# Performance work log

Hardware: AMD Instinct MI355X
Metric: run time of the kernel (lower is better)

Reference implementation:

```python
import jax, jax.numpy as jnp
import numpy as np

NODE_IN = 128
NODE_OUT = 128
LEAKY_SLOPE = 0.01  # torch nn.LeakyReLU default


def setup_inputs() -> dict:
    key = jax.random.key(0)
    k1, k2, k3, k4 = jax.random.split(key, 4)
    B, N = 64, 1024
    node_mat = jax.random.normal(k1, (B, N, NODE_IN), dtype=jnp.float32)
    adj_mat = jax.random.uniform(k2, (B, N, N), dtype=jnp.float32)
    # Linear(node_in_len, node_out_len): W [out, in], b [out] (torch default init style)
    bound = 1.0 / np.sqrt(NODE_IN)
    W = jax.random.uniform(k3, (NODE_OUT, NODE_IN), minval=-bound, maxval=bound, dtype=jnp.float32)
    b = jax.random.uniform(k4, (NODE_OUT,), minval=-bound, maxval=bound, dtype=jnp.float32)
    return {"node_mat": node_mat, "adj_mat": adj_mat, "W": W, "b": b}


def reference(node_mat, adj_mat, W, b):
    # n_neighbors[b,i] = sum_j adj[b,i,j]; diag(1/deg) @ adj == adj / deg (row-wise)
    deg = jnp.sum(adj_mat, axis=-1, keepdims=True)          # [B,N,1]
    norm_adj = adj_mat / deg                                 # [B,N,N]
    agg = jnp.einsum('bij,bjf->bif', norm_adj, node_mat)     # [B,N,Fin]
    out = jnp.einsum('bif,of->bio', agg, W) + b              # [B,N,Fout]
    return jnp.where(out >= 0, out, LEAKY_SLOPE * out)
```

## Files before the change

### kernel.cpp

```cpp
#include <hip/hip_runtime.h>
#include <hip/hip_bf16.h>


typedef __attribute__((ext_vector_type(8))) short bf16x8;
typedef __attribute__((ext_vector_type(4))) float f32x4;

__device__ __forceinline__ unsigned f2bf(float x) {
  unsigned u = __builtin_bit_cast(unsigned, x);
  u += 0x7FFFu + ((u >> 16) & 1u);
  return u >> 16;
}
__device__ __forceinline__ int f2bf2(float x, float y) {
  return (int)(f2bf(x) | (f2bf(y) << 16));
}

#define JPAD 136
#define KP   72

__global__ __launch_bounds__(256) void k_ht(const float* __restrict__ node,
                                            const float* __restrict__ W,
                                            ushort* __restrict__ Ht) {
  __shared__ short nt[128 * JPAD];
  __shared__ short wt[128 * JPAD];
  const int b = blockIdx.y, jt = blockIdx.x, t = threadIdx.x;
  const float4* nbase = (const float4*)(node + (size_t)(b * 1024 + jt * 128) * 128);
  const float4* wbase = (const float4*)W;

  #pragma unroll
  for (int p = 0; p < 16; p++) {
    int idx = t + 256 * p;
    int r = idx >> 5, c4 = idx & 31;
    float4 v = nbase[idx];
    int2 s; s.x = f2bf2(v.x, v.y); s.y = f2bf2(v.z, v.w);
    *(int2*)&nt[r * JPAD + c4 * 4] = s;
    float4 wv = wbase[idx];
    int2 sw; sw.x = f2bf2(wv.x, wv.y); sw.y = f2bf2(wv.z, wv.w);
    *(int2*)&wt[r * JPAD + c4 * 4] = sw;
  }
  __syncthreads();

  const int lane = t & 63, wid = t >> 6;
  const int q = lane >> 4, r = lane & 15;
  const int wm = wid & 1, wn = wid >> 1;
  f32x4 acc[4][4] = {};
  #pragma unroll
  for (int ks = 0; ks < 4; ks++) {
    bf16x8 af[4], bg[4];
    #pragma unroll
    for (int mi = 0; mi < 4; mi++)
      af[mi] = *(const bf16x8*)&nt[(wm * 64 + mi * 16 + r) * JPAD + ks * 32 + q * 8];
    #pragma unroll
    for (int ni = 0; ni < 4; ni++)
      bg[ni] = *(const bf16x8*)&wt[(wn * 64 + ni * 16 + r) * JPAD + ks * 32 + q * 8];
    #pragma unroll
    for (int mi = 0; mi < 4; mi++)
      #pragma unroll
      for (int ni = 0; ni < 4; ni++)
        acc[mi][ni] = __builtin_amdgcn_mfma_f32_16x16x32_bf16(af[mi], bg[ni], acc[mi][ni], 0, 0, 0);
  }
  __syncthreads();

  #pragma unroll
  for (int mi = 0; mi < 4; mi++)
    #pragma unroll
    for (int ni = 0; ni < 4; ni++)
      #pragma unroll
      for (int v = 0; v < 4; v++) {
        int j = wm * 64 + mi * 16 + q * 4 + v;
        int o = wn * 64 + ni * 16 + r;
        nt[o * JPAD + j] = (short)f2bf(acc[mi][ni][v]);
      }
  __syncthreads();
  {
    int o = t >> 1, half = t & 1;
    const int4* src = (const int4*)&nt[o * JPAD + half * 64];
    int4* dst = (int4*)(Ht + (size_t)b * 131072 + (size_t)o * 1024 + jt * 128 + half * 64);
    #pragma unroll
    for (int i = 0; i < 8; i++) dst[i] = src[i];
  }
}

__global__ __launch_bounds__(256) void k_main(const float* __restrict__ adj,
                                              const ushort* __restrict__ Ht,
                                              const float* __restrict__ bias,
                                              float* __restrict__ out) {
  __shared__ short at[128 * KP];
  __shared__ short ht[128 * KP];
  __shared__ float deg[128];
  const int b = blockIdx.y, it = blockIdx.x, t = threadIdx.x;
  const float4* abase = (const float4*)(adj + (size_t)(b * 1024 + it * 128) * 1024);
  const int4* hbase = (const int4*)(Ht + (size_t)b * 131072);
  const int lane = t & 63, wid = t >> 6;
  const int q = lane >> 4, r = lane & 15;
  const int wm = wid & 1, wn = wid >> 1;
  const int arow = t >> 4, ac4 = t & 15;
  const int hrow = t >> 3, hc8 = t & 7;
  f32x4 acc[4][4] = {};
  float rs[8] = {0, 0, 0, 0, 0, 0, 0, 0};
  float bias_r[4];
  #pragma unroll
  for (int ni = 0; ni < 4; ni++) bias_r[ni] = bias[wn * 64 + ni * 16 + r];

  for (int kt = 0; kt < 16; kt++) {
    float4 av[8];
    #pragma unroll
    for (int p = 0; p < 8; p++)
      av[p] = abase[(size_t)(arow + 16 * p) * 256 + kt * 16 + ac4];
    int4 hv[4];
    #pragma unroll
    for (int p = 0; p < 4; p++)
      hv[p] = hbase[(size_t)(hrow + 32 * p) * 128 + kt * 8 + hc8];
    __syncthreads();
    #pragma unroll
    for (int p = 0; p < 8; p++) {
      rs[p] += (av[p].x + av[p].y) + (av[p].z + av[p].w);
      int2 s; s.x = f2bf2(av[p].x, av[p].y); s.y = f2bf2(av[p].z, av[p].w);
      *(int2*)&at[(arow + 16 * p) * KP + ac4 * 4] = s;
    }
    #pragma unroll
    for (int p = 0; p < 4; p++)
      *(int4*)&ht[(hrow + 32 * p) * KP + hc8 * 8] = hv[p];
    __syncthreads();
    #pragma unroll
    for (int ks = 0; ks < 2; ks++) {
      bf16x8 af[4], bg[4];
      #pragma unroll
      for (int mi = 0; mi < 4; mi++)
        af[mi] = *(const bf16x8*)&at[(wm * 64 + mi * 16 + r) * KP + ks * 32 + q * 8];
      #pragma unroll
      for (int ni = 0; ni < 4; ni++)
        bg[ni] = *(const bf16x8*)&ht[(wn * 64 + ni * 16 + r) * KP + ks * 32 + q * 8];
      #pragma unroll
      for (int mi = 0; mi < 4; mi++)
        #pragma unroll
        for (int ni = 0; ni < 4; ni++)
          acc[mi][ni] = __builtin_amdgcn_mfma_f32_16x16x32_bf16(af[mi], bg[ni], acc[mi][ni], 0, 0, 0);
    }
  }

  #pragma unroll
  for (int p = 0; p < 8; p++) {
    float v = rs[p];
    v += __shfl_down(v, 8, 16);
    v += __shfl_down(v, 4, 16);
    v += __shfl_down(v, 2, 16);
    v += __shfl_down(v, 1, 16);
    rs[p] = v;
  }
  if ((t & 15) == 0) {
    #pragma unroll
    for (int p = 0; p < 8; p++) deg[arow + 16 * p] = rs[p];
  }
  __syncthreads();

  float* obase = out + (size_t)(b * 1024 + it * 128) * 128;
  #pragma unroll
  for (int mi = 0; mi < 4; mi++)
    #pragma unroll
    for (int v = 0; v < 4; v++) {
      int i = wm * 64 + mi * 16 + q * 4 + v;
      float rd = 1.0f / deg[i];
      #pragma unroll
      for (int ni = 0; ni < 4; ni++) {
        int o = wn * 64 + ni * 16 + r;
        float val = acc[mi][ni][v] * rd + bias_r[ni];
        val = val >= 0.0f ? val : 0.01f * val;
        obase[(size_t)i * 128 + o] = val;
      }
    }
}

__global__ __launch_bounds__(256) void k_fallback(const float* __restrict__ node,
                                                  const float* __restrict__ adj,
                                                  const float* __restrict__ W,
                                                  const float* __restrict__ bias,
                                                  float* __restrict__ out) {
  __shared__ float red[256];
  __shared__ float agg[128];
  const int b = blockIdx.y, i = blockIdx.x, t = threadIdx.x;
  const float* arow = adj + (size_t)(b * 1024 + i) * 1024;
  float s = 0.f;
  for (int j = t; j < 1024; j += 256) s += arow[j];
  red[t] = s;
  __syncthreads();
  if (t < 128) red[t] += red[t + 128];
  __syncthreads();
  if (t < 64) {
    float v2 = red[t] + red[t + 64];
    #pragma unroll
    for (int off = 32; off; off >>= 1) v2 += __shfl_down(v2, off);
    if (t == 0) red[0] = v2;
  }
  __syncthreads();
  const float rdeg = 1.0f / red[0];
  const int f = t & 127, half = t >> 7;
  const float* nb = node + (size_t)b * 1024 * 128;
  float a = 0.f;
  for (int j = half * 512; j < half * 512 + 512; j++)
    a += arow[j] * nb[(size_t)j * 128 + f];
  __syncthreads();
  if (half == 0) agg[f] = a;
  __syncthreads();
  if (half == 1) agg[f] += a;
  __syncthreads();
  if (t < 128) {
    const float* wr = W + t * 128;
    float o = 0.f;
    for (int f2 = 0; f2 < 128; f2++) o += agg[f2] * wr[f2];
    o = o * rdeg + bias[t];
    out[(size_t)(b * 1024 + i) * 128 + t] = o >= 0.f ? o : 0.01f * o;
  }
}

extern "C" void kernel_launch(void* const* d_in, const int* in_sizes, int n_in,
                              void* d_out, int out_size, void* d_ws, size_t ws_size,
                              hipStream_t stream) {
  const float* node = (const float*)d_in[0];
  const float* adj  = (const float*)d_in[1];
  const float* W    = (const float*)d_in[2];
  const float* bias = (const float*)d_in[3];
  float* out = (float*)d_out;
  const size_t ht_bytes = (size_t)64 * 128 * 1024 * 2;
  if (ws_size >= ht_bytes) {
    ushort* Ht = (ushort*)d_ws;
    k_ht<<<dim3(8, 64), 256, 0, stream>>>(node, W, Ht);
    k_main<<<dim3(8, 64), 256, 0, stream>>>(adj, Ht, bias, out);
  } else {
    k_fallback<<<dim3(1024, 64), 256, 0, stream>>>(node, adj, W, bias, out);
  }
}
```

Measured before the change: 424.2 us.

## Restructure aggregation kernel to stream adj and H straight into MFMA registers

The main kernel drops LDS staging entirely. Each wave now owns 16 adjacency rows across all 128 output features and loads its bf16-converted adj fragments directly as MFMA A operands, with the next K tile prefetched into registers. H fragments are read straight from global/L2 for each wave, and row degrees are reduced with cross-lane shuffles instead of LDS. The grid doubles to 1024 blocks. This removes the __syncthreads and LDS round trips, but each wave re-reads the full H slice from cache, which sharply raises L2 traffic.

```diff
diff --git a/kernel.cpp b/kernel.cpp
--- a/kernel.cpp
+++ b/kernel.cpp
@@ -15,7 +15,6 @@
 }
 
 #define JPAD 136
-#define KP   72
 
 __global__ __launch_bounds__(256) void k_ht(const float* __restrict__ node,
                                             const float* __restrict__ W,
@@ -84,90 +83,65 @@
                                               const ushort* __restrict__ Ht,
                                               const float* __restrict__ bias,
                                               float* __restrict__ out) {
-  __shared__ short at[128 * KP];
-  __shared__ short ht[128 * KP];
-  __shared__ float deg[128];
   const int b = blockIdx.y, it = blockIdx.x, t = threadIdx.x;
-  const float4* abase = (const float4*)(adj + (size_t)(b * 1024 + it * 128) * 1024);
-  const int4* hbase = (const int4*)(Ht + (size_t)b * 131072);
   const int lane = t & 63, wid = t >> 6;
   const int q = lane >> 4, r = lane & 15;
-  const int wm = wid & 1, wn = wid >> 1;
-  const int arow = t >> 4, ac4 = t & 15;
-  const int hrow = t >> 3, hc8 = t & 7;
-  f32x4 acc[4][4] = {};
-  float rs[8] = {0, 0, 0, 0, 0, 0, 0, 0};
-  float bias_r[4];
-  #pragma unroll
-  for (int ni = 0; ni < 4; ni++) bias_r[ni] = bias[wn * 64 + ni * 16 + r];
-
+  const int i0 = it * 64 + wid * 16;
+  const float4* ap = (const float4*)(adj + (size_t)(b * 1024 + i0 + r) * 1024);
+  const int4* hb = (const int4*)(Ht + (size_t)b * 131072) + r * 128;
+
+  f32x4 acc[8] = {};
+  float rs = 0.f;
+
+  float4 a0 = ap[q * 2], a1 = ap[q * 2 + 1], a2 = ap[q * 2 + 8], a3 = ap[q * 2 + 9];
+
+  #pragma unroll 1
   for (int kt = 0; kt < 16; kt++) {
-    float4 av[8];
-    #pragma unroll
-    for (int p = 0; p < 8; p++)
-      av[p] = abase[(size_t)(arow + 16 * p) * 256 + kt * 16 + ac4];
-    int4 hv[4];
-    #pragma unroll
-    for (int p = 0; p < 4; p++)
-      hv[p] = hbase[(size_t)(hrow + 32 * p) * 128 + kt * 8 + hc8];
-    __syncthreads();
-    #pragma unroll
-    for (int p = 0; p < 8; p++) {
-      rs[p] += (av[p].x + av[p].y) + (av[p].z + av[p].w);
-      int2 s; s.x = f2bf2(av[p].x, av[p].y); s.y = f2bf2(av[p].z, av[p].w);
-      *(int2*)&at[(arow + 16 * p) * KP + ac4 * 4] = s;
+    int4 bv[8];
+    #pragma unroll
+    for (int ni = 0; ni < 8; ni++) bv[ni] = hb[ni * 2048 + kt * 8 + q];
+
+    union { bf16x8 v; int i[4]; } u0, u1;
+    u0.i[0] = f2bf2(a0.x, a0.y); u0.i[1] = f2bf2(a0.z, a0.w);
+    u0.i[2] = f2bf2(a1.x, a1.y); u0.i[3] = f2bf2(a1.z, a1.w);
+    u1.i[0] = f2bf2(a2.x, a2.y); u1.i[1] = f2bf2(a2.z, a2.w);
+    u1.i[2] = f2bf2(a3.x, a3.y); u1.i[3] = f2bf2(a3.z, a3.w);
+    rs += (a0.x + a0.y + a0.z + a0.w) + (a1.x + a1.y + a1.z + a1.w)
+        + (a2.x + a2.y + a2.z + a2.w) + (a3.x + a3.y + a3.z + a3.w);
+
+    const int nb = (kt < 15 ? kt + 1 : 15) * 16 + q * 2;
+    float4 n0 = ap[nb], n1 = ap[nb + 1], n2 = ap[nb + 8], n3 = ap[nb + 9];
+
+    #pragma unroll
+    for (int ni = 0; ni < 8; ni++)
+      acc[ni] = __builtin_amdgcn_mfma_f32_16x16x32_bf16(
+          u0.v, __builtin_bit_cast(bf16x8, bv[ni]), acc[ni], 0, 0, 0);
+
+    #pragma unroll
+    for (int ni = 0; ni < 8; ni++) bv[ni] = hb[ni * 2048 + kt * 8 + 4 + q];
+    #pragma unroll
+    for (int ni = 0; ni < 8; ni++)
+      acc[ni] = __builtin_amdgcn_mfma_f32_16x16x32_bf16(
+          u1.v, __builtin_bit_cast(bf16x8, bv[ni]), acc[ni], 0, 0, 0);
+
+    a0 = n0; a1 = n1; a2 = n2; a3 = n3;
+  }
+
+  rs += __shfl_xor(rs, 16);
+  rs += __shfl_xor(rs, 32);
+
+  float* obase = out + (size_t)(b * 1024 + i0) * 128;
+  #pragma unroll
+  for (int v = 0; v < 4; v++) {
+    const float rd = 1.0f / __shfl(rs, q * 4 + v);
+    const int i = q * 4 + v;
+    #pragma unroll
+    for (int ni = 0; ni < 8; ni++) {
+      float val = acc[ni][v] * rd + bias[ni * 16 + r];
+      val = val >= 0.0f ? val : 0.01f * val;
+      obase[(size_t)i * 128 + ni * 16 + r] = val;
     }
-    #pragma unroll
-    for (int p = 0; p < 4; p++)
-      *(int4*)&ht[(hrow + 32 * p) * KP + hc8 * 8] = hv[p];
-    __syncthreads();
-    #pragma unroll
-    for (int ks = 0; ks < 2; ks++) {
-      bf16x8 af[4], bg[4];
-      #pragma unroll
-      for (int mi = 0; mi < 4; mi++)
-        af[mi] = *(const bf16x8*)&at[(wm * 64 + mi * 16 + r) * KP + ks * 32 + q * 8];
-      #pragma unroll
-      for (int ni = 0; ni < 4; ni++)
-        bg[ni] = *(const bf16x8*)&ht[(wn * 64 + ni * 16 + r) * KP + ks * 32 + q * 8];
-      #pragma unroll
-      for (int mi = 0; mi < 4; mi++)
-        #pragma unroll
-        for (int ni = 0; ni < 4; ni++)
-          acc[mi][ni] = __builtin_amdgcn_mfma_f32_16x16x32_bf16(af[mi], bg[ni], acc[mi][ni], 0, 0, 0);
-    }
-  }
-
-  #pragma unroll
-  for (int p = 0; p < 8; p++) {
-    float v = rs[p];
-    v += __shfl_down(v, 8, 16);
-    v += __shfl_down(v, 4, 16);
-    v += __shfl_down(v, 2, 16);
-    v += __shfl_down(v, 1, 16);
-    rs[p] = v;
-  }
-  if ((t & 15) == 0) {
-    #pragma unroll
-    for (int p = 0; p < 8; p++) deg[arow + 16 * p] = rs[p];
-  }
-  __syncthreads();
-
-  float* obase = out + (size_t)(b * 1024 + it * 128) * 128;
-  #pragma unroll
-  for (int mi = 0; mi < 4; mi++)
-    #pragma unroll
-    for (int v = 0; v < 4; v++) {
-      int i = wm * 64 + mi * 16 + q * 4 + v;
-      float rd = 1.0f / deg[i];
-      #pragma unroll
-      for (int ni = 0; ni < 4; ni++) {
-        int o = wn * 64 + ni * 16 + r;
-        float val = acc[mi][ni][v] * rd + bias_r[ni];
-        val = val >= 0.0f ? val : 0.01f * val;
-        obase[(size_t)i * 128 + o] = val;
-      }
-    }
+  }
 }
 
 __global__ __launch_bounds__(256) void k_fallback(const float* __restrict__ node,
@@ -224,7 +198,7 @@
   if (ws_size >= ht_bytes) {
     ushort* Ht = (ushort*)d_ws;
     k_ht<<<dim3(8, 64), 256, 0, stream>>>(node, W, Ht);
-    k_main<<<dim3(8, 64), 256, 0, stream>>>(adj, Ht, bias, out);
+    k_main<<<dim3(16, 64), 256, 0, stream>>>(adj, Ht, bias, out);
   } else {
     k_fallback<<<dim3(1024, 64), 256, 0, stream>>>(node, adj, W, bias, out);
   }
```

Result: slower. 469.8 us (+10.7%).
